# Kernel tuning notes

Measured on AMD Instinct MI355X. Metric: run time of the kernel, lower is better.

## Reference

```python
import jax, jax.numpy as jnp
import numpy as np

NUM_GRAPHS = 128

def setup_inputs() -> dict:
    key = jax.random.key(0)
    ks = jax.random.split(key, 12)
    N, E = 50000, 800000
    x = jax.random.normal(ks[0], (N, 54), dtype=jnp.float32)
    edge_index = jax.random.randint(ks[1], (2, E), 0, N, dtype=jnp.int64)
    batch = jnp.sort(jax.random.randint(ks[2], (N,), 0, NUM_GRAPHS, dtype=jnp.int64))
    def lin(k, fi, fo):
        return jax.random.normal(k, (fi, fo), dtype=jnp.float32) / np.sqrt(fi)
    return {
        "x": x, "edge_index": edge_index, "batch": batch,
        "W1l": lin(ks[3], 54, 128), "b1": jnp.zeros((128,), jnp.float32), "W1r": lin(ks[4], 54, 128),
        "W2l": lin(ks[5], 128, 256), "b2": jnp.zeros((256,), jnp.float32), "W2r": lin(ks[6], 128, 256),
        "W3l": lin(ks[7], 256, 256), "b3": jnp.zeros((256,), jnp.float32), "W3r": lin(ks[8], 256, 256),
    }

def _sage(h, src, dst, n, Wl, b, Wr):
    # sum-aggregate neighbor features x_j (j=src) into node i (i=dst), then
    # out = lin_l(agg) + lin_r(h)  (PyG SAGEConv, aggr='sum')
    agg = jax.ops.segment_sum(h[src], dst, num_segments=n)
    return jax.nn.relu(agg @ Wl + b + h @ Wr)

def reference(x, edge_index, batch, W1l, b1, W1r, W2l, b2, W2r, W3l, b3, W3r):
    n = x.shape[0]
    src, dst = edge_index[0], edge_index[1]
    h = _sage(x, src, dst, n, W1l, b1, W1r)
    h = _sage(h, src, dst, n, W2l, b2, W2r)
    h = _sage(h, src, dst, n, W3l, b3, W3r)
    # global mean pool per graph (gep = global_mean_pool)
    sums = jax.ops.segment_sum(h, batch, num_segments=NUM_GRAPHS)
    cnts = jax.ops.segment_sum(jnp.ones((n, 1), h.dtype), batch, num_segments=NUM_GRAPHS)
    return sums / jnp.maximum(cnts, 1.0)
```

## Files before the change

### kernel.cpp

```cpp
#include <hip/hip_runtime.h>


typedef unsigned short u16;
typedef __attribute__((ext_vector_type(8))) short bf16x8;
typedef __attribute__((ext_vector_type(4))) float f32x4;

__device__ __forceinline__ u16 f2b(float f) {
    union { float f; unsigned u; } v; v.f = f;
    unsigned u = v.u;
    return (u16)((u + 0x7FFF + ((u >> 16) & 1)) >> 16);
}
__device__ __forceinline__ float b2f(u16 h) {
    union { unsigned u; float f; } v; v.u = ((unsigned)h) << 16;
    return v.f;
}
__device__ __forceinline__ float blo(unsigned u) {
    union { unsigned u; float f; } v; v.u = u << 16;
    return v.f;
}
__device__ __forceinline__ float bhi(unsigned u) {
    union { unsigned u; float f; } v; v.u = u & 0xffff0000u;
    return v.f;
}

__global__ void k_prep(const float* __restrict__ x,
                       const float* __restrict__ W1l, const float* __restrict__ W1r,
                       const float* __restrict__ W2l, const float* __restrict__ W2r,
                       const float* __restrict__ W3l, const float* __restrict__ W3r,
                       u16* __restrict__ xb,
                       u16* __restrict__ wt1l, u16* __restrict__ wt1r,
                       u16* __restrict__ wt2l, u16* __restrict__ wt2r,
                       u16* __restrict__ wt3l, u16* __restrict__ wt3r, int N) {
    long idx = (long)blockIdx.x * 256 + threadIdx.x;
    long s0 = (long)N * 54;
    if (idx < s0) { xb[idx] = f2b(x[idx]); return; }
    idx -= s0;
    if (idx < 2 * 128 * 64) {
        u16* o = (idx < 128 * 64) ? wt1l : wt1r;
        const float* w = (idx < 128 * 64) ? W1l : W1r;
        long loc = idx % (128 * 64);
        int d = (int)(loc >> 6), k = (int)(loc & 63);
        o[loc] = (k < 54) ? f2b(w[(long)k * 128 + d]) : 0;
        return;
    }
    idx -= 2 * 128 * 64;
    if (idx < 2 * 256 * 128) {
        u16* o = (idx < 256 * 128) ? wt2l : wt2r;
        const float* w = (idx < 256 * 128) ? W2l : W2r;
        long loc = idx % (256 * 128);
        int d = (int)(loc >> 7), k = (int)(loc & 127);
        o[loc] = f2b(w[(long)k * 256 + d]);
        return;
    }
    idx -= 2 * 256 * 128;
    if (idx < 2 * 256 * 256) {
        u16* o = (idx < 256 * 256) ? wt3l : wt3r;
        const float* w = (idx < 256 * 256) ? W3l : W3r;
        long loc = idx % (256 * 256);
        int d = (int)(loc >> 8), k = (int)(loc & 255);
        o[loc] = f2b(w[(long)k * 256 + d]);
    }
}

__global__ void k_count(const int* __restrict__ dst, int* __restrict__ cnt, int E) {
    int e = blockIdx.x * 256 + threadIdx.x;
    if (e < E) atomicAdd(&cnt[dst[e]], 1);
}

__global__ void k_bsum(const int* __restrict__ cnt, int* __restrict__ bsum, int N) {
    __shared__ int sm[256];
    int i = blockIdx.x * 256 + threadIdx.x;
    sm[threadIdx.x] = (i < N) ? cnt[i] : 0;
    __syncthreads();
    for (int off = 128; off > 0; off >>= 1) {
        if (threadIdx.x < off) sm[threadIdx.x] += sm[threadIdx.x + off];
        __syncthreads();
    }
    if (threadIdx.x == 0) bsum[blockIdx.x] = sm[0];
}

__global__ void k_bscan(const int* __restrict__ bsum, int* __restrict__ boff, int NB) {
    __shared__ int sm[256];
    int t = threadIdx.x;
    int v = (t < NB) ? bsum[t] : 0;
    sm[t] = v;
    __syncthreads();
    for (int off = 1; off < 256; off <<= 1) {
        int add = (t >= off) ? sm[t - off] : 0;
        __syncthreads();
        sm[t] += add;
        __syncthreads();
    }
    if (t < NB) boff[t] = sm[t] - v;
}

__global__ void k_scan(const int* __restrict__ cnt, const int* __restrict__ boff,
                       int* __restrict__ rowptr, int* __restrict__ wpos, int N, int E) {
    __shared__ int sm[256];
    int t = threadIdx.x;
    int i = blockIdx.x * 256 + t;
    int v = (i < N) ? cnt[i] : 0;
    sm[t] = v;
    __syncthreads();
    for (int off = 1; off < 256; off <<= 1) {
        int add = (t >= off) ? sm[t - off] : 0;
        __syncthreads();
        sm[t] += add;
        __syncthreads();
    }
    int ex = sm[t] - v + boff[blockIdx.x];
    if (i < N) { rowptr[i] = ex; wpos[i] = ex; }
    if (i == 0) rowptr[N] = E;
}

__global__ void k_fill(const int* __restrict__ src, const int* __restrict__ dst,
                       int* __restrict__ wpos, int* __restrict__ csr, int E) {
    int e = blockIdx.x * 256 + threadIdx.x;
    if (e < E) {
        int p = atomicAdd(&wpos[dst[e]], 1);
        csr[p] = src[e];
    }
}

__global__ __launch_bounds__(256) void k_agg54(const u16* __restrict__ h,
                                               const int* __restrict__ rowptr,
                                               const int* __restrict__ csr,
                                               u16* __restrict__ agg, int n) {
    constexpr int D = 54;
    int w = threadIdx.x >> 6;
    int lane = threadIdx.x & 63;
    int i = blockIdx.x * 4 + w;
    if (i >= n) return;
    int b0 = rowptr[i], b1 = rowptr[i + 1];
    if (lane < D) {
        float a0 = 0.f;
        #pragma unroll 8
        for (int b = b0; b < b1; ++b) {
            int s = csr[b];
            a0 += b2f(h[(size_t)s * D + lane]);
        }
        agg[(size_t)i * D + lane] = f2b(a0);
    }
}

template <int D, int EPW>
__global__ __launch_bounds__(256) void k_aggv(const u16* __restrict__ h,
                                              const int* __restrict__ rowptr,
                                              const int* __restrict__ csr,
                                              u16* __restrict__ agg, int n) {
    constexpr int GRP = 64 / EPW;
    static_assert(D == GRP * 8, "geometry");
    int w = threadIdx.x >> 6;
    int lane = threadIdx.x & 63;
    int i = blockIdx.x * 4 + w;
    if (i >= n) return;
    int b0 = rowptr[i], b1 = rowptr[i + 1];
    int sub = lane / GRP;
    int dl = lane % GRP;

    float a0 = 0.f, a1 = 0.f, a2 = 0.f, a3 = 0.f;
    float a4 = 0.f, a5 = 0.f, a6 = 0.f, a7 = 0.f;

    int b = b0;
    #pragma unroll 4
    for (; b + EPW <= b1; b += EPW) {
        int s = csr[b + sub];
        uint4 v = *reinterpret_cast<const uint4*>(h + (size_t)s * D + dl * 8);
        a0 += blo(v.x); a1 += bhi(v.x);
        a2 += blo(v.y); a3 += bhi(v.y);
        a4 += blo(v.z); a5 += bhi(v.z);
        a6 += blo(v.w); a7 += bhi(v.w);
    }
    int rem = b1 - b;
    if (sub < rem) {
        int s = csr[b + sub];
        uint4 v = *reinterpret_cast<const uint4*>(h + (size_t)s * D + dl * 8);
        a0 += blo(v.x); a1 += bhi(v.x);
        a2 += blo(v.y); a3 += bhi(v.y);
        a4 += blo(v.z); a5 += bhi(v.z);
        a6 += blo(v.w); a7 += bhi(v.w);
    }
    #pragma unroll
    for (int off = GRP; off < 64; off <<= 1) {
        a0 += __shfl_xor(a0, off, 64);
        a1 += __shfl_xor(a1, off, 64);
        a2 += __shfl_xor(a2, off, 64);
        a3 += __shfl_xor(a3, off, 64);
        a4 += __shfl_xor(a4, off, 64);
        a5 += __shfl_xor(a5, off, 64);
        a6 += __shfl_xor(a6, off, 64);
        a7 += __shfl_xor(a7, off, 64);
    }
    if (sub == 0) {
        uint4 o;
        o.x = ((unsigned)f2b(a0)) | (((unsigned)f2b(a1)) << 16);
        o.y = ((unsigned)f2b(a2)) | (((unsigned)f2b(a3)) << 16);
        o.z = ((unsigned)f2b(a4)) | (((unsigned)f2b(a5)) << 16);
        o.w = ((unsigned)f2b(a6)) | (((unsigned)f2b(a7)) << 16);
        *reinterpret_cast<uint4*>(agg + (size_t)i * D + dl * 8) = o;
    }
}

template <int KA, int KW, int DOUT, bool A16>
__global__ __launch_bounds__(256) void k_mgemm(const u16* __restrict__ A1,
                                               const u16* __restrict__ A2,
                                               const u16* __restrict__ Wt1,
                                               const u16* __restrict__ Wt2,
                                               const float* __restrict__ bias,
                                               u16* __restrict__ C, int N) {
    constexpr int BM = 128, BKP = 40;
    __shared__ u16 As[BM * BKP];
    __shared__ u16 Bs[BM * BKP];

    const int tid = threadIdx.x;
    const int w = tid >> 6, l = tid & 63;
    const int wr = w >> 1, wc = w & 1;
    const int lo = l & 15, hi = l >> 4;
    const int m0 = blockIdx.x * BM;
    const int n0 = 0;

    f32x4 acc[4][4];
    #pragma unroll
    for (int i = 0; i < 4; ++i)
        #pragma unroll
        for (int j = 0; j < 4; ++j) acc[i][j] = {0.f, 0.f, 0.f, 0.f};

    constexpr int KT = KW / 32;

    #pragma unroll
    for (int s = 0; s < 2; ++s) {
        const u16* __restrict__ Ap = s ? A2 : A1;
        const u16* __restrict__ Wp = s ? Wt2 : Wt1;
        for (int kt = 0; kt < KT; ++kt) {
            const int k0 = kt * 32;
            #pragma unroll
            for (int it = 0; it < 2; ++it) {
                int v = it * 256 + tid;
                int r = v >> 2, c = v & 3;
                uint4 val = *reinterpret_cast<const uint4*>(Wp + (size_t)(n0 + r) * KW + k0 + c * 8);
                *reinterpret_cast<uint4*>(&Bs[r * BKP + c * 8]) = val;
            }
            if constexpr (A16) {
                #pragma unroll
                for (int it = 0; it < 2; ++it) {
                    int v = it * 256 + tid;
                    int r = v >> 2, c = v & 3;
                    int m = m0 + r;
                    uint4 val = {0u, 0u, 0u, 0u};
                    if (m < N) val = *reinterpret_cast<const uint4*>(Ap + (size_t)m * KA + k0 + c * 8);
                    *reinterpret_cast<uint4*>(&As[r * BKP + c * 8]) = val;
                }
            } else {
                #pragma unroll
                for (int it = 0; it < 8; ++it) {
                    int v = it * 256 + tid;
                    int r = v >> 4, c = v & 15;
                    int m = m0 + r;
                    int k = k0 + c * 2;
                    unsigned val = 0;
                    if (m < N && k < KA)
                        val = *reinterpret_cast<const unsigned*>(Ap + (size_t)m * KA + k);
                    *reinterpret_cast<unsigned*>(&As[r * BKP + c * 2]) = val;
                }
            }
            __syncthreads();
            bf16x8 af[4], bf[4];
            #pragma unroll
            for (int f = 0; f < 4; ++f) {
                af[f] = *reinterpret_cast<const bf16x8*>(&Bs[(wc * 64 + f * 16 + lo) * BKP + hi * 8]);
                bf[f] = *reinterpret_cast<const bf16x8*>(&As[(wr * 64 + f * 16 + lo) * BKP + hi * 8]);
            }
            #pragma unroll
            for (int fm = 0; fm < 4; ++fm)
                #pragma unroll
                for (int fn = 0; fn < 4; ++fn)
                    acc[fm][fn] = __builtin_amdgcn_mfma_f32_16x16x32_bf16(af[fn], bf[fm], acc[fm][fn], 0, 0, 0);
            __syncthreads();
        }
    }
    #pragma unroll
    for (int fm = 0; fm < 4; ++fm) {
        int node = m0 + wr * 64 + fm * 16 + lo;
        if (node < N) {
            #pragma unroll
            for (int fn = 0; fn < 4; ++fn) {
                int fb = n0 + wc * 64 + fn * 16 + hi * 4;
                float4 bv = *reinterpret_cast<const float4*>(bias + fb);
                ushort4 o;
                o.x = f2b(fmaxf(acc[fm][fn][0] + bv.x, 0.f));
                o.y = f2b(fmaxf(acc[fm][fn][1] + bv.y, 0.f));
                o.z = f2b(fmaxf(acc[fm][fn][2] + bv.z, 0.f));
                o.w = f2b(fmaxf(acc[fm][fn][3] + bv.w, 0.f));
                *reinterpret_cast<ushort4*>(C + (size_t)node * DOUT + fb) = o;
            }
        }
    }
}

template <int KA, int DOUT>
__global__ __launch_bounds__(512) void k_mgemm2(const u16* __restrict__ A1,
                                                const u16* __restrict__ A2,
                                                const u16* __restrict__ Wt1,
                                                const u16* __restrict__ Wt2,
                                                const float* __restrict__ bias,
                                                u16* __restrict__ C, int N) {
    constexpr int BM = 64, BKP = 40;
    constexpr int WCOL = DOUT / 4;
    constexpr int FN = WCOL / 16;
    __shared__ u16 As[BM * BKP];
    __shared__ u16 Bs[DOUT * BKP];

    const int tid = threadIdx.x;
    const int w = tid >> 6, lane = tid & 63;
    const int wr = w >> 2, wc = w & 3;
    const int lo = lane & 15, hi = lane >> 4;
    const int m0 = blockIdx.x * BM;

    f32x4 acc[2][FN];
    #pragma unroll
    for (int i = 0; i < 2; ++i)
        #pragma unroll
        for (int j = 0; j < FN; ++j) acc[i][j] = {0.f, 0.f, 0.f, 0.f};

    constexpr int KT = KA / 32;

    #pragma unroll
    for (int s = 0; s < 2; ++s) {
        const u16* __restrict__ Ap = s ? A2 : A1;
        const u16* __restrict__ Wp = s ? Wt2 : Wt1;
        for (int kt = 0; kt < KT; ++kt) {
            const int k0 = kt * 32;
            #pragma unroll
            for (int it = 0; it < DOUT * 32 / 8 / 512; ++it) {
                int v = it * 512 + tid;
                int r = v >> 2, c = v & 3;
                uint4 val = *reinterpret_cast<const uint4*>(Wp + (size_t)r * KA + k0 + c * 8);
                *reinterpret_cast<uint4*>(&Bs[r * BKP + c * 8]) = val;
            }
            if (tid < 256) {
                int r = tid >> 2, c = tid & 3;
                int m = m0 + r;
                uint4 val = {0u, 0u, 0u, 0u};
                if (m < N) val = *reinterpret_cast<const uint4*>(Ap + (size_t)m * KA + k0 + c * 8);
                *reinterpret_cast<uint4*>(&As[r * BKP + c * 8]) = val;
            }
            __syncthreads();
            bf16x8 bfr[2];
            #pragma unroll
            for (int fm = 0; fm < 2; ++fm)
                bfr[fm] = *reinterpret_cast<const bf16x8*>(&As[(wr * 32 + fm * 16 + lo) * BKP + hi * 8]);
            #pragma unroll
            for (int fn = 0; fn < FN; ++fn) {
                bf16x8 af = *reinterpret_cast<const bf16x8*>(&Bs[(wc * WCOL + fn * 16 + lo) * BKP + hi * 8]);
                #pragma unroll
                for (int fm = 0; fm < 2; ++fm)
                    acc[fm][fn] = __builtin_amdgcn_mfma_f32_16x16x32_bf16(af, bfr[fm], acc[fm][fn], 0, 0, 0);
            }
            __syncthreads();
        }
    }
    #pragma unroll
    for (int fm = 0; fm < 2; ++fm) {
        int node = m0 + wr * 32 + fm * 16 + lo;
        if (node < N) {
            #pragma unroll
            for (int fn = 0; fn < FN; ++fn) {
                int fb = wc * WCOL + fn * 16 + hi * 4;
                float4 bv = *reinterpret_cast<const float4*>(bias + fb);
                ushort4 o;
                o.x = f2b(fmaxf(acc[fm][fn][0] + bv.x, 0.f));
                o.y = f2b(fmaxf(acc[fm][fn][1] + bv.y, 0.f));
                o.z = f2b(fmaxf(acc[fm][fn][2] + bv.z, 0.f));
                o.w = f2b(fmaxf(acc[fm][fn][3] + bv.w, 0.f));
                *reinterpret_cast<ushort4*>(C + (size_t)node * DOUT + fb) = o;
            }
        }
    }
}

template <int ROWS>
__global__ void k_pool(const u16* __restrict__ h3, const int* __restrict__ batch,
                       float* __restrict__ outsum, int* __restrict__ cnt, int N) {
    int r0 = blockIdx.x * ROWS;
    int r1 = min(r0 + ROWS, N);
    if (r0 >= N) return;
    int d = threadIdx.x;
    int cur = batch[r0];
    float s = 0.f;
    int c = 0;
    for (int i = r0; i < r1; ++i) {
        int g = batch[i];
        if (g != cur) {
            atomicAdd(&outsum[cur * 256 + d], s);
            if (d == 0) atomicAdd(&cnt[cur], c);
            s = 0.f; c = 0; cur = g;
        }
        s += b2f(h3[(size_t)i * 256 + d]);
        c++;
    }
    atomicAdd(&outsum[cur * 256 + d], s);
    if (d == 0) atomicAdd(&cnt[cur], c);
}

__global__ void k_div(float* __restrict__ out, const int* __restrict__ cnt, int total) {
    int idx = blockIdx.x * 256 + threadIdx.x;
    if (idx < total) {
        float c = fmaxf((float)cnt[idx >> 8], 1.0f);
        out[idx] = out[idx] / c;
    }
}

extern "C" void kernel_launch(void* const* d_in, const int* in_sizes, int n_in,
                              void* d_out, int out_size, void* d_ws, size_t ws_size,
                              hipStream_t stream) {
    const float* x   = (const float*)d_in[0];
    const int* ei    = (const int*)d_in[1];
    const int* batch = (const int*)d_in[2];
    const float* W1l = (const float*)d_in[3];
    const float* b1  = (const float*)d_in[4];
    const float* W1r = (const float*)d_in[5];
    const float* W2l = (const float*)d_in[6];
    const float* b2  = (const float*)d_in[7];
    const float* W2r = (const float*)d_in[8];
    const float* W3l = (const float*)d_in[9];
    const float* b3  = (const float*)d_in[10];
    const float* W3r = (const float*)d_in[11];

    const int N = in_sizes[0] / 54;
    const int E = in_sizes[1] / 2;
    const int* src = ei;
    const int* dst = ei + E;

    u16* xb   = (u16*)d_ws;
    u16* bufA = xb + (size_t)N * 54;
    u16* buf1 = bufA + (size_t)N * 256;
    u16* buf2 = buf1 + (size_t)N * 256;
    u16* wt1l = buf2 + (size_t)N * 256;
    u16* wt1r = wt1l + 128 * 64;
    u16* wt2l = wt1r + 128 * 64;
    u16* wt2r = wt2l + 256 * 128;
    u16* wt3l = wt2r + 256 * 128;
    u16* wt3r = wt3l + 256 * 256;
    int* ip = (int*)(wt3r + 256 * 256);
    int* cntdeg  = ip; ip += N;
    int* rowptr  = ip; ip += N + 1;
    int* wpos    = ip; ip += N + 1;
    int* bsum    = ip; ip += 256;
    int* boff    = ip; ip += 256;
    int* cntpool = ip; ip += 128;
    int* csr     = ip;

    hipMemsetAsync(cntdeg, 0, (size_t)N * sizeof(int), stream);
    hipMemsetAsync(d_out, 0, (size_t)out_size * sizeof(float), stream);
    hipMemsetAsync(cntpool, 0, 128 * sizeof(int), stream);

    const int NB = (N + 255) / 256;
    const int EB = (E + 255) / 256;

    {
        long total = (long)N * 54 + 2L * 128 * 64 + 2L * 256 * 128 + 2L * 256 * 256;
        int g = (int)((total + 255) / 256);
        k_prep<<<g, 256, 0, stream>>>(x, W1l, W1r, W2l, W2r, W3l, W3r,
                                      xb, wt1l, wt1r, wt2l, wt2r, wt3l, wt3r, N);
    }

    k_count<<<EB, 256, 0, stream>>>(dst, cntdeg, E);
    k_bsum<<<NB, 256, 0, stream>>>(cntdeg, bsum, N);
    k_bscan<<<1, 256, 0, stream>>>(bsum, boff, NB);
    k_scan<<<NB, 256, 0, stream>>>(cntdeg, boff, rowptr, wpos, N, E);
    k_fill<<<EB, 256, 0, stream>>>(src, dst, wpos, csr, E);

    const int AGB = (N + 3) / 4;
    const int GX = (N + 127) / 128;
    const int GX2 = (N + 63) / 64;

    k_agg54<<<AGB, 256, 0, stream>>>(xb, rowptr, csr, bufA, N);
    k_mgemm<54, 64, 128, false><<<GX, 256, 0, stream>>>(bufA, xb, wt1l, wt1r, b1, buf1, N);
    k_aggv<128, 4><<<AGB, 256, 0, stream>>>(buf1, rowptr, csr, bufA, N);
    k_mgemm2<128, 256><<<GX2, 512, 0, stream>>>(bufA, buf1, wt2l, wt2r, b2, buf2, N);
    k_aggv<256, 2><<<AGB, 256, 0, stream>>>(buf2, rowptr, csr, bufA, N);
    k_mgemm2<256, 256><<<GX2, 512, 0, stream>>>(bufA, buf2, wt3l, wt3r, b3, buf1, N);

    k_pool<32><<<(N + 31) / 32, 256, 0, stream>>>(buf1, batch, (float*)d_out, cntpool, N);
    k_div<<<(out_size + 255) / 256, 256, 0, stream>>>((float*)d_out, cntpool, out_size);
}
```

Measured before the change: 342.9 us.

## Split layer-3 aggregation into XCC-affine column chunks via atomic work counters

Replaces the layer-3 neighbor aggregation with a kernel that splits the 256-wide feature into 8 column chunks of 32. Each block reads its XCC ID and atomically claims node groups from a per-chunk counter, so that blocks on one XCC mostly gather the same column slice. The aim is for each XCC's L2 to cache a narrower working set of the gathered rows, giving better locality for the random gathers. In exchange it launches 8x more blocks with atomic dispatch overhead, does each 16-byte gather separately per chunk, and re-reads rowptr/csr eight times.

```diff
diff --git a/kernel.cpp b/kernel.cpp
--- a/kernel.cpp
+++ b/kernel.cpp
@@ -198,6 +198,85 @@
         o.z = ((unsigned)f2b(a4)) | (((unsigned)f2b(a5)) << 16);
         o.w = ((unsigned)f2b(a6)) | (((unsigned)f2b(a7)) << 16);
         *reinterpret_cast<uint4*>(agg + (size_t)i * D + dl * 8) = o;
+    }
+}
+
+template <int D, int CF>
+__global__ __launch_bounds__(256) void k_aggx(const u16* __restrict__ h,
+                                              const int* __restrict__ rowptr,
+                                              const int* __restrict__ csr,
+                                              u16* __restrict__ agg,
+                                              int* __restrict__ ctr,
+                                              int ngrp, int n) {
+    static_assert(D == CF * 8, "8 chunks");
+    constexpr int LPE = CF / 8;
+    constexpr int SLOTS = 64 / LPE;
+
+    __shared__ int s_item[2];
+    if (threadIdx.x == 0) {
+        unsigned xcc;
+        asm volatile("s_getreg_b32 %0, hwreg(HW_REG_XCC_ID)" : "=s"(xcc));
+        int grp = -1, chunk = 0;
+        #pragma unroll 1
+        for (int t = 0; t < 8; ++t) {
+            int c = (int)((xcc + t) & 7u);
+            int g = atomicAdd(&ctr[c], 1);
+            if (g < ngrp) { grp = g; chunk = c; break; }
+        }
+        s_item[0] = grp; s_item[1] = chunk;
+    }
+    __syncthreads();
+    const int grp = s_item[0], chunk = s_item[1];
+    if (grp < 0) return;
+
+    const int w = threadIdx.x >> 6, lane = threadIdx.x & 63;
+    const int slot = lane / LPE;
+    const int fl = lane % LPE;
+    const int col = chunk * CF + fl * 8;
+
+    for (int t = 0; t < 8; ++t) {
+        int node = grp * 32 + w * 8 + t;
+        if (node >= n) continue;
+        int b0 = __builtin_nontemporal_load(&rowptr[node]);
+        int b1 = __builtin_nontemporal_load(&rowptr[node + 1]);
+        float a0 = 0.f, a1 = 0.f, a2 = 0.f, a3 = 0.f;
+        float a4 = 0.f, a5 = 0.f, a6 = 0.f, a7 = 0.f;
+        int b = b0;
+        for (; b + SLOTS <= b1; b += SLOTS) {
+            int s = __builtin_nontemporal_load(&csr[b + slot]);
+            uint4 v = *reinterpret_cast<const uint4*>(h + (size_t)s * D + col);
+            a0 += blo(v.x); a1 += bhi(v.x);
+            a2 += blo(v.y); a3 += bhi(v.y);
+            a4 += blo(v.z); a5 += bhi(v.z);
+            a6 += blo(v.w); a7 += bhi(v.w);
+        }
+        if (slot < b1 - b) {
+            int s = __builtin_nontemporal_load(&csr[b + slot]);
+            uint4 v = *reinterpret_cast<const uint4*>(h + (size_t)s * D + col);
+            a0 += blo(v.x); a1 += bhi(v.x);
+            a2 += blo(v.y); a3 += bhi(v.y);
+            a4 += blo(v.z); a5 += bhi(v.z);
+            a6 += blo(v.w); a7 += bhi(v.w);
+        }
+        #pragma unroll
+        for (int off = LPE; off < 64; off <<= 1) {
+            a0 += __shfl_xor(a0, off, 64);
+            a1 += __shfl_xor(a1, off, 64);
+            a2 += __shfl_xor(a2, off, 64);
+            a3 += __shfl_xor(a3, off, 64);
+            a4 += __shfl_xor(a4, off, 64);
+            a5 += __shfl_xor(a5, off, 64);
+            a6 += __shfl_xor(a6, off, 64);
+            a7 += __shfl_xor(a7, off, 64);
+        }
+        if (slot == 0) {
+            uint4 o;
+            o.x = ((unsigned)f2b(a0)) | (((unsigned)f2b(a1)) << 16);
+            o.y = ((unsigned)f2b(a2)) | (((unsigned)f2b(a3)) << 16);
+            o.z = ((unsigned)f2b(a4)) | (((unsigned)f2b(a5)) << 16);
+            o.w = ((unsigned)f2b(a6)) | (((unsigned)f2b(a7)) << 16);
+            *reinterpret_cast<uint4*>(agg + (size_t)node * D + col) = o;
+        }
     }
 }
 
@@ -448,11 +527,13 @@
     int* bsum    = ip; ip += 256;
     int* boff    = ip; ip += 256;
     int* cntpool = ip; ip += 128;
+    int* ctrx    = ip; ip += 8;
     int* csr     = ip;
 
     hipMemsetAsync(cntdeg, 0, (size_t)N * sizeof(int), stream);
     hipMemsetAsync(d_out, 0, (size_t)out_size * sizeof(float), stream);
     hipMemsetAsync(cntpool, 0, 128 * sizeof(int), stream);
+    hipMemsetAsync(ctrx, 0, 8 * sizeof(int), stream);
 
     const int NB = (N + 255) / 256;
     const int EB = (E + 255) / 256;
@@ -478,7 +559,10 @@
     k_mgemm<54, 64, 128, false><<<GX, 256, 0, stream>>>(bufA, xb, wt1l, wt1r, b1, buf1, N);
     k_aggv<128, 4><<<AGB, 256, 0, stream>>>(buf1, rowptr, csr, bufA, N);
     k_mgemm2<128, 256><<<GX2, 512, 0, stream>>>(bufA, buf1, wt2l, wt2r, b2, buf2, N);
-    k_aggv<256, 2><<<AGB, 256, 0, stream>>>(buf2, rowptr, csr, bufA, N);
+    {
+        int ngrp = (N + 31) / 32;
+        k_aggx<256, 32><<<8 * ngrp, 256, 0, stream>>>(buf2, rowptr, csr, bufA, ctrx, ngrp, N);
+    }
     k_mgemm2<256, 256><<<GX2, 512, 0, stream>>>(bufA, buf2, wt3l, wt3r, b3, buf1, N);
 
     k_pool<32><<<(N + 31) / 32, 256, 0, stream>>>(buf1, batch, (float*)d_out, cntpool, N);
```

Result: slower. 480.4 us (+40.1%).

## Pad layer-1 features to 64 and fold degree counting into prep kernel

Applied to the files above, without the earlier changes.

The bf16 copy of x is padded from 54 to 64 columns with zeros. This lets layer 1 use the vectorized aggregation kernel (8 edges per wave, 16-byte loads) and the aligned GEMM path in place of the scalar per-lane gather. The in-degree atomic count is also merged into the prep kernel, which removes one launch. Padding adds about 18% more bytes per gathered row, and the atomics now share a grid with the conversion work.

```diff
diff --git a/kernel.cpp b/kernel.cpp
--- a/kernel.cpp
+++ b/kernel.cpp
@@ -27,13 +27,19 @@
                        const float* __restrict__ W1l, const float* __restrict__ W1r,
                        const float* __restrict__ W2l, const float* __restrict__ W2r,
                        const float* __restrict__ W3l, const float* __restrict__ W3r,
+                       const int* __restrict__ dst, int* __restrict__ cntdeg,
                        u16* __restrict__ xb,
                        u16* __restrict__ wt1l, u16* __restrict__ wt1r,
                        u16* __restrict__ wt2l, u16* __restrict__ wt2r,
-                       u16* __restrict__ wt3l, u16* __restrict__ wt3r, int N) {
+                       u16* __restrict__ wt3l, u16* __restrict__ wt3r,
+                       int N, int E) {
     long idx = (long)blockIdx.x * 256 + threadIdx.x;
-    long s0 = (long)N * 54;
-    if (idx < s0) { xb[idx] = f2b(x[idx]); return; }
+    long s0 = (long)N * 64;
+    if (idx < s0) {
+        int row = (int)(idx >> 6), k = (int)(idx & 63);
+        xb[idx] = (k < 54) ? f2b(x[(size_t)row * 54 + k]) : 0;
+        return;
+    }
     idx -= s0;
     if (idx < 2 * 128 * 64) {
         u16* o = (idx < 128 * 64) ? wt1l : wt1r;
@@ -59,12 +65,10 @@
         long loc = idx % (256 * 256);
         int d = (int)(loc >> 8), k = (int)(loc & 255);
         o[loc] = f2b(w[(long)k * 256 + d]);
-    }
-}
-
-__global__ void k_count(const int* __restrict__ dst, int* __restrict__ cnt, int E) {
-    int e = blockIdx.x * 256 + threadIdx.x;
-    if (e < E) atomicAdd(&cnt[dst[e]], 1);
+        return;
+    }
+    idx -= 2 * 256 * 256;
+    if (idx < E) atomicAdd(&cntdeg[dst[idx]], 1);
 }
 
 __global__ void k_bsum(const int* __restrict__ cnt, int* __restrict__ bsum, int N) {
@@ -119,27 +123,6 @@
     if (e < E) {
         int p = atomicAdd(&wpos[dst[e]], 1);
         csr[p] = src[e];
-    }
-}
-
-__global__ __launch_bounds__(256) void k_agg54(const u16* __restrict__ h,
-                                               const int* __restrict__ rowptr,
-                                               const int* __restrict__ csr,
-                                               u16* __restrict__ agg, int n) {
-    constexpr int D = 54;
-    int w = threadIdx.x >> 6;
-    int lane = threadIdx.x & 63;
-    int i = blockIdx.x * 4 + w;
-    if (i >= n) return;
-    int b0 = rowptr[i], b1 = rowptr[i + 1];
-    if (lane < D) {
-        float a0 = 0.f;
-        #pragma unroll 8
-        for (int b = b0; b < b1; ++b) {
-            int s = csr[b];
-            a0 += b2f(h[(size_t)s * D + lane]);
-        }
-        agg[(size_t)i * D + lane] = f2b(a0);
     }
 }
 
@@ -432,7 +415,7 @@
     const int* dst = ei + E;
 
     u16* xb   = (u16*)d_ws;
-    u16* bufA = xb + (size_t)N * 54;
+    u16* bufA = xb + (size_t)N * 64;
     u16* buf1 = bufA + (size_t)N * 256;
     u16* buf2 = buf1 + (size_t)N * 256;
     u16* wt1l = buf2 + (size_t)N * 256;
@@ -458,13 +441,13 @@
     const int EB = (E + 255) / 256;
 
     {
-        long total = (long)N * 54 + 2L * 128 * 64 + 2L * 256 * 128 + 2L * 256 * 256;
+        long total = (long)N * 64 + 2L * 128 * 64 + 2L * 256 * 128 + 2L * 256 * 256 + E;
         int g = (int)((total + 255) / 256);
         k_prep<<<g, 256, 0, stream>>>(x, W1l, W1r, W2l, W2r, W3l, W3r,
-                                      xb, wt1l, wt1r, wt2l, wt2r, wt3l, wt3r, N);
-    }
-
-    k_count<<<EB, 256, 0, stream>>>(dst, cntdeg, E);
+                                      dst, cntdeg,
+                                      xb, wt1l, wt1r, wt2l, wt2r, wt3l, wt3r, N, E);
+    }
+
     k_bsum<<<NB, 256, 0, stream>>>(cntdeg, bsum, N);
     k_bscan<<<1, 256, 0, stream>>>(bsum, boff, NB);
     k_scan<<<NB, 256, 0, stream>>>(cntdeg, boff, rowptr, wpos, N, E);
@@ -474,8 +457,8 @@
     const int GX = (N + 127) / 128;
     const int GX2 = (N + 63) / 64;
 
-    k_agg54<<<AGB, 256, 0, stream>>>(xb, rowptr, csr, bufA, N);
-    k_mgemm<54, 64, 128, false><<<GX, 256, 0, stream>>>(bufA, xb, wt1l, wt1r, b1, buf1, N);
+    k_aggv<64, 8><<<AGB, 256, 0, stream>>>(xb, rowptr, csr, bufA, N);
+    k_mgemm<64, 64, 128, true><<<GX, 256, 0, stream>>>(bufA, xb, wt1l, wt1r, b1, buf1, N);
     k_aggv<128, 4><<<AGB, 256, 0, stream>>>(buf1, rowptr, csr, bufA, N);
     k_mgemm2<128, 256><<<GX2, 512, 0, stream>>>(bufA, buf1, wt2l, wt2r, b2, buf2, N);
     k_aggv<256, 2><<<AGB, 256, 0, stream>>>(buf2, rowptr, csr, bufA, N);
```

Result: faster. 304.3 us, median of 2 (-11.3%).
